# Kernel optimization log

Measured on AMD Instinct MI355X. Metric: run time of the kernel, lower is better.

Reference implementation:

```python
import jax, jax.numpy as jnp
import numpy as np

LN_EPS = 1e-5
B, N, D, V = 2048, 8, 1024, 4096


def setup_inputs() -> dict:
    key = jax.random.key(0)
    k1, k2, k3, k4 = jax.random.split(key, 4)
    return {
        "input_embedding": jax.random.normal(k1, (B, D), dtype=jnp.float32),
        "features": jax.random.randint(k2, (B, N), 0, V, dtype=jnp.int64),
        "embed_tables": jax.random.normal(k3, (N, V, D), dtype=jnp.float32) * 0.02,
        "W_pred": jax.random.normal(k4, (N, D, V), dtype=jnp.float32) * 0.02,
        "b_pred": jnp.zeros((N, V), dtype=jnp.float32),
        "ln_gamma": jnp.ones((D,), dtype=jnp.float32),
        "ln_beta": jnp.zeros((D,), dtype=jnp.float32),
    }


def reference(input_embedding, features, embed_tables, W_pred, b_pred, ln_gamma, ln_beta):
    # Per-feature embedding lookup: embed_tables[n, features[b,n]] -> [B, N, D]
    feat_emb = embed_tables[jnp.arange(N)[None, :], features]
    # Stack input embedding in front: [B, N+1, D]
    embeddings = jnp.concatenate([input_embedding[:, None, :], feat_emb], axis=1)
    # Original: triu(diag=1) mask-multiply-sum then [:, 1:, :].
    # masked_sums[:, t] = sum_{s < t} emb[:, s]; slicing t=1..N == inclusive cumsum
    # over the first N positions.
    masked_sums = jnp.cumsum(embeddings, axis=1)[:, :-1, :]  # [B, N, D]
    # LayerNorm over last dim
    mu = jnp.mean(masked_sums, axis=-1, keepdims=True)
    var = jnp.var(masked_sums, axis=-1, keepdims=True)
    h = (masked_sums - mu) / jnp.sqrt(var + LN_EPS) * ln_gamma + ln_beta
    # Exact (erf) GELU, matching nn.GELU default
    h = jax.nn.gelu(h, approximate=False)
    # Per-feature predictor heads as one batched GEMM: [B, N, V]
    logits = jnp.einsum("bnd,ndv->bnv", h, W_pred) + b_pred
    return logits
```

## Files before the change

### kernel.cpp

```cpp
#include <hip/hip_runtime.h>
#include <hip/hip_bf16.h>

#define B_ 2048
#define N_ 8
#define D_ 1024
#define V_ 4096
#define LN_EPS_ 1e-5f

typedef __bf16 bf16x8 __attribute__((ext_vector_type(8)));
typedef float f32x4 __attribute__((ext_vector_type(4)));

#define GLB(p) ((const __attribute__((address_space(1))) void*)(p))
#define LDSP(p) ((__attribute__((address_space(3))) void*)(p))

static __device__ __forceinline__ unsigned short f2bf(float x) {
    union { float f; unsigned int u; } v;
    v.f = x;
    unsigned int r = v.u + 0x7fffu + ((v.u >> 16) & 1u);
    return (unsigned short)(r >> 16);
}

__global__ __launch_bounds__(256) void wconv(const float* __restrict__ W,
                                             unsigned short* __restrict__ Wt) {
    __shared__ unsigned short tile[64][65];
    const int n  = blockIdx.z;
    const int v0 = blockIdx.x * 64;
    const int d0 = blockIdx.y * 64;
    const int tx = threadIdx.x;
    const int ty = threadIdx.y;
#pragma unroll
    for (int i = 0; i < 4; ++i) {
        const int d = ty + i * 16;
        const float4 w4 = *(const float4*)&W[((size_t)n * D_ + d0 + d) * V_ + v0 + tx * 4];
        tile[d][tx * 4 + 0] = f2bf(w4.x);
        tile[d][tx * 4 + 1] = f2bf(w4.y);
        tile[d][tx * 4 + 2] = f2bf(w4.z);
        tile[d][tx * 4 + 3] = f2bf(w4.w);
    }
    __syncthreads();
#pragma unroll
    for (int i = 0; i < 4; ++i) {
        const int v = ty + i * 16;
        ushort4 pk;
        pk.x = tile[tx * 4 + 0][v];
        pk.y = tile[tx * 4 + 1][v];
        pk.z = tile[tx * 4 + 2][v];
        pk.w = tile[tx * 4 + 3][v];
        *reinterpret_cast<ushort4*>(&Wt[((size_t)n * V_ + v0 + v) * D_ + d0 + tx * 4]) = pk;
    }
}

__global__ __launch_bounds__(256) void stage1(const float* __restrict__ ie,
                                              const int* __restrict__ feats,
                                              const float* __restrict__ emb,
                                              const float* __restrict__ gamma,
                                              const float* __restrict__ beta,
                                              unsigned short* __restrict__ H) {
    const int b = blockIdx.x;
    const int t = threadIdx.x;
    const int d0 = t * 4;
    const int lane = t & 63, wid = t >> 6;

    float4 s  = *(const float4*)&ie[(size_t)b * D_ + d0];
    const float4 g4 = *(const float4*)&gamma[d0];
    const float4 be4 = *(const float4*)&beta[d0];

    int fc[N_];
#pragma unroll
    for (int n = 0; n < N_; ++n) fc[n] = feats[b * N_ + n];

    __shared__ float redS[4], redQ[4];

#pragma unroll
    for (int n = 0; n < N_; ++n) {
        float ls = s.x + s.y + s.z + s.w;
        float lq = s.x * s.x + s.y * s.y + s.z * s.z + s.w * s.w;
#pragma unroll
        for (int off = 32; off > 0; off >>= 1) {
            ls += __shfl_down(ls, off, 64);
            lq += __shfl_down(lq, off, 64);
        }
        if (lane == 0) { redS[wid] = ls; redQ[wid] = lq; }
        __syncthreads();
        const float tot  = redS[0] + redS[1] + redS[2] + redS[3];
        const float totq = redQ[0] + redQ[1] + redQ[2] + redQ[3];
        __syncthreads();

        const float mu   = tot * (1.0f / D_);
        const float var  = totq * (1.0f / D_) - mu * mu;
        const float rstd = rsqrtf(var + LN_EPS_);

        float h0 = (s.x - mu) * rstd * g4.x + be4.x;
        float h1 = (s.y - mu) * rstd * g4.y + be4.y;
        float h2 = (s.z - mu) * rstd * g4.z + be4.z;
        float h3 = (s.w - mu) * rstd * g4.w + be4.w;
        h0 = 0.5f * h0 * (1.0f + erff(h0 * 0.70710678f));
        h1 = 0.5f * h1 * (1.0f + erff(h1 * 0.70710678f));
        h2 = 0.5f * h2 * (1.0f + erff(h2 * 0.70710678f));
        h3 = 0.5f * h3 * (1.0f + erff(h3 * 0.70710678f));

        ushort4 pk;
        pk.x = f2bf(h0); pk.y = f2bf(h1); pk.z = f2bf(h2); pk.w = f2bf(h3);
        *reinterpret_cast<ushort4*>(&H[((size_t)n * B_ + b) * D_ + d0]) = pk;

        const float4 e = *(const float4*)&emb[((size_t)n * V_ + fc[n]) * (size_t)D_ + d0];
        s.x += e.x; s.y += e.y; s.z += e.z; s.w += e.w;
    }
}

#define MF(a, b, c) __builtin_amdgcn_mfma_f32_16x16x32_bf16((a), (b), (c), 0, 0, 0)

#define STG_A(u, kt, bb) __builtin_amdgcn_global_load_lds( \
    GLB(Ab + (size_t)((u) * 64 + srow) * D_ + (kt) + gsl), \
    LDSP(lds + (bb) + (u) * 8192 + t * 16), 16, 0, 0)
#define STG_B(u, kt, bb) __builtin_amdgcn_global_load_lds( \
    GLB(Bb + (size_t)((u) * 64 + srow) * D_ + (kt) + gsl), \
    LDSP(lds + (bb) + 32768 + (u) * 8192 + t * 16), 16, 0, 0)

#define RD_A(i, ks, bb) (*(const bf16x8*)(lds + (bb) + ((i) >> 1) * 8192 + \
    (((i) & 1) * 32 + wr * 16 + lrow) * 128 + ((((ks) * 4 + lkq) ^ sw) * 16)))
#define RD_B(j, ks, bb) (*(const bf16x8*)(lds + (bb) + 32768 + wc * 8192 + \
    ((j) * 16 + lrow) * 128 + ((((ks) * 4 + lkq) ^ sw) * 16)))

#define QUADP(i0, i1) \
    _Pragma("unroll") for (int j = 0; j < 4; ++j) { \
        acc[i0][j] = MF(A00, Bf[j][0], acc[i0][j]); \
        acc[i0][j] = MF(A01, Bf[j][1], acc[i0][j]); \
        acc[i1][j] = MF(A10, Bf[j][0], acc[i1][j]); \
        acc[i1][j] = MF(A11, Bf[j][1], acc[i1][j]); \
    }

#define TILE(KT, bc, bn) { \
    bf16x8 Bf[4][2]; \
    asm volatile("s_waitcnt vmcnt(3)" ::: "memory"); \
    __builtin_amdgcn_s_barrier(); \
    _Pragma("unroll") for (int j = 0; j < 4; ++j) { Bf[j][0] = RD_B(j, 0, bc); Bf[j][1] = RD_B(j, 1, bc); } \
    { bf16x8 A00 = RD_A(0, 0, bc), A01 = RD_A(0, 1, bc), A10 = RD_A(1, 0, bc), A11 = RD_A(1, 1, bc); \
      STG_B(0, (KT) + 64, bn); STG_B(1, (KT) + 64, bn); \
      __builtin_amdgcn_s_setprio(1); QUADP(0, 1); __builtin_amdgcn_s_setprio(0); } \
    asm volatile("s_waitcnt vmcnt(4)" ::: "memory"); \
    __builtin_amdgcn_s_barrier(); \
    { bf16x8 A00 = RD_A(2, 0, bc), A01 = RD_A(2, 1, bc), A10 = RD_A(3, 0, bc), A11 = RD_A(3, 1, bc); \
      STG_B(2, (KT) + 64, bn); STG_B(3, (KT) + 64, bn); \
      __builtin_amdgcn_s_setprio(1); QUADP(2, 3); __builtin_amdgcn_s_setprio(0); } \
    asm volatile("s_waitcnt vmcnt(4)" ::: "memory"); \
    __builtin_amdgcn_s_barrier(); \
    { bf16x8 A00 = RD_A(4, 0, bc), A01 = RD_A(4, 1, bc), A10 = RD_A(5, 0, bc), A11 = RD_A(5, 1, bc); \
      STG_A(0, (KT) + 64, bn); STG_A(1, (KT) + 64, bn); \
      __builtin_amdgcn_s_setprio(1); QUADP(4, 5); __builtin_amdgcn_s_setprio(0); } \
    asm volatile("s_waitcnt vmcnt(6)" ::: "memory"); \
    __builtin_amdgcn_s_barrier(); \
    { bf16x8 A00 = RD_A(6, 0, bc), A01 = RD_A(6, 1, bc), A10 = RD_A(7, 0, bc), A11 = RD_A(7, 1, bc); \
      STG_A(2, (KT) + 64, bn); STG_A(3, (KT) + 64, bn); \
      __builtin_amdgcn_s_setprio(1); QUADP(6, 7); __builtin_amdgcn_s_setprio(0); } \
}

#define TILE_LAST(bc) { \
    bf16x8 Bf[4][2]; \
    asm volatile("s_waitcnt vmcnt(3)" ::: "memory"); \
    __builtin_amdgcn_s_barrier(); \
    _Pragma("unroll") for (int j = 0; j < 4; ++j) { Bf[j][0] = RD_B(j, 0, bc); Bf[j][1] = RD_B(j, 1, bc); } \
    { bf16x8 A00 = RD_A(0, 0, bc), A01 = RD_A(0, 1, bc), A10 = RD_A(1, 0, bc), A11 = RD_A(1, 1, bc); \
      __builtin_amdgcn_s_setprio(1); QUADP(0, 1); __builtin_amdgcn_s_setprio(0); } \
    asm volatile("s_waitcnt vmcnt(2)" ::: "memory"); \
    __builtin_amdgcn_s_barrier(); \
    { bf16x8 A00 = RD_A(2, 0, bc), A01 = RD_A(2, 1, bc), A10 = RD_A(3, 0, bc), A11 = RD_A(3, 1, bc); \
      __builtin_amdgcn_s_setprio(1); QUADP(2, 3); __builtin_amdgcn_s_setprio(0); } \
    asm volatile("s_waitcnt vmcnt(1)" ::: "memory"); \
    __builtin_amdgcn_s_barrier(); \
    { bf16x8 A00 = RD_A(4, 0, bc), A01 = RD_A(4, 1, bc), A10 = RD_A(5, 0, bc), A11 = RD_A(5, 1, bc); \
      __builtin_amdgcn_s_setprio(1); QUADP(4, 5); __builtin_amdgcn_s_setprio(0); } \
    asm volatile("s_waitcnt vmcnt(0)" ::: "memory"); \
    __builtin_amdgcn_s_barrier(); \
    { bf16x8 A00 = RD_A(6, 0, bc), A01 = RD_A(6, 1, bc), A10 = RD_A(7, 0, bc), A11 = RD_A(7, 1, bc); \
      __builtin_amdgcn_s_setprio(1); QUADP(6, 7); __builtin_amdgcn_s_setprio(0); } \
}

__global__ __launch_bounds__(512, 2) void gemm8(const unsigned short* __restrict__ H,
                                                const unsigned short* __restrict__ Wt,
                                                const float* __restrict__ bp,
                                                float* __restrict__ out) {
    extern __shared__ char lds[];
    const int vt = blockIdx.x, mt = blockIdx.y, n = blockIdx.z;
    const int t = threadIdx.x;
    const int wid = t >> 6, lane = t & 63;
    const int wr = wid >> 2, wc = wid & 3;

    const unsigned short* Ab = H  + ((size_t)n * B_ + (size_t)mt * 256) * D_;
    const unsigned short* Bb = Wt + ((size_t)n * V_ + (size_t)vt * 256) * D_;

    const int srow = t >> 3;
    const int gsl  = ((t & 7) ^ (srow & 7)) * 8;

    const int lrow = lane & 15;
    const int lkq  = lane >> 4;
    const int sw   = lane & 7;

    f32x4 acc[8][4] = {};

    STG_B(0, 0, 0); STG_B(1, 0, 0); STG_B(2, 0, 0); STG_B(3, 0, 0);
    STG_A(0, 0, 0); STG_A(1, 0, 0); STG_A(2, 0, 0); STG_A(3, 0, 0);

    int kt = 0;
#pragma unroll 1
    for (int it = 0; it < 7; ++it) {
        TILE(kt, 0, 65536); kt += 64;
        TILE(kt, 65536, 0); kt += 64;
    }
    TILE(kt, 0, 65536);
    TILE_LAST(65536);

    const int col = lane & 15;
    const int rg  = (lane >> 4) * 4;
    const int gc0 = vt * 256 + wc * 64 + col;
    float bias[4];
#pragma unroll
    for (int j = 0; j < 4; ++j) bias[j] = bp[(size_t)n * V_ + gc0 + j * 16];
#pragma unroll
    for (int i = 0; i < 8; ++i) {
        const int row = mt * 256 + i * 32 + wr * 16 + rg;
#pragma unroll
        for (int j = 0; j < 4; ++j) {
            const int gcol = gc0 + j * 16;
#pragma unroll
            for (int r = 0; r < 4; ++r) {
                out[((size_t)(row + r) * N_ + n) * V_ + gcol] = acc[i][j][r] + bias[j];
            }
        }
    }
}

extern "C" void kernel_launch(void* const* d_in, const int* in_sizes, int n_in,
                              void* d_out, int out_size, void* d_ws, size_t ws_size,
                              hipStream_t stream) {
    const float* ie  = (const float*)d_in[0];
    const int*   fts = (const int*)d_in[1];
    const float* emb = (const float*)d_in[2];
    const float* W   = (const float*)d_in[3];
    const float* bp  = (const float*)d_in[4];
    const float* gam = (const float*)d_in[5];
    const float* bet = (const float*)d_in[6];
    float* out = (float*)d_out;

    unsigned short* Wt = (unsigned short*)d_ws;
    unsigned short* H  = (unsigned short*)((char*)d_ws + (size_t)N_ * V_ * D_ * 2);

    (void)hipFuncSetAttribute(reinterpret_cast<const void*>(gemm8),
                              hipFuncAttributeMaxDynamicSharedMemorySize, 131072);

    wconv<<<dim3(V_ / 64, D_ / 64, N_), dim3(16, 16), 0, stream>>>(W, Wt);
    stage1<<<dim3(B_), dim3(256), 0, stream>>>(ie, fts, emb, gam, bet, H);
    gemm8<<<dim3(V_ / 256, B_ / 256, N_), 512, 131072, stream>>>(H, Wt, bp, out);
}
```

Baseline: 254.0 us.

## Merge prep kernels and make GEMM blocks persistent across four V tiles

Result: slower. 340.7 us (+34.1%).

```diff
diff --git a/kernel.cpp b/kernel.cpp
--- a/kernel.cpp
+++ b/kernel.cpp
@@ -20,101 +20,103 @@
     return (unsigned short)(r >> 16);
 }
 
-__global__ __launch_bounds__(256) void wconv(const float* __restrict__ W,
-                                             unsigned short* __restrict__ Wt) {
-    __shared__ unsigned short tile[64][65];
-    const int n  = blockIdx.z;
-    const int v0 = blockIdx.x * 64;
-    const int d0 = blockIdx.y * 64;
-    const int tx = threadIdx.x;
-    const int ty = threadIdx.y;
-#pragma unroll
-    for (int i = 0; i < 4; ++i) {
-        const int d = ty + i * 16;
-        const float4 w4 = *(const float4*)&W[((size_t)n * D_ + d0 + d) * V_ + v0 + tx * 4];
-        tile[d][tx * 4 + 0] = f2bf(w4.x);
-        tile[d][tx * 4 + 1] = f2bf(w4.y);
-        tile[d][tx * 4 + 2] = f2bf(w4.z);
-        tile[d][tx * 4 + 3] = f2bf(w4.w);
-    }
-    __syncthreads();
-#pragma unroll
-    for (int i = 0; i < 4; ++i) {
-        const int v = ty + i * 16;
-        ushort4 pk;
-        pk.x = tile[tx * 4 + 0][v];
-        pk.y = tile[tx * 4 + 1][v];
-        pk.z = tile[tx * 4 + 2][v];
-        pk.w = tile[tx * 4 + 3][v];
-        *reinterpret_cast<ushort4*>(&Wt[((size_t)n * V_ + v0 + v) * D_ + d0 + tx * 4]) = pk;
-    }
-}
-
-__global__ __launch_bounds__(256) void stage1(const float* __restrict__ ie,
-                                              const int* __restrict__ feats,
-                                              const float* __restrict__ emb,
-                                              const float* __restrict__ gamma,
-                                              const float* __restrict__ beta,
-                                              unsigned short* __restrict__ H) {
-    const int b = blockIdx.x;
+__global__ __launch_bounds__(256) void prep(const float* __restrict__ ie,
+                                            const int* __restrict__ feats,
+                                            const float* __restrict__ emb,
+                                            const float* __restrict__ gamma,
+                                            const float* __restrict__ beta,
+                                            const float* __restrict__ W,
+                                            unsigned short* __restrict__ H,
+                                            unsigned short* __restrict__ Wt) {
+    const int bid = blockIdx.x;
     const int t = threadIdx.x;
-    const int d0 = t * 4;
-    const int lane = t & 63, wid = t >> 6;
-
-    float4 s  = *(const float4*)&ie[(size_t)b * D_ + d0];
-    const float4 g4 = *(const float4*)&gamma[d0];
-    const float4 be4 = *(const float4*)&beta[d0];
-
-    int fc[N_];
-#pragma unroll
-    for (int n = 0; n < N_; ++n) fc[n] = feats[b * N_ + n];
-
-    __shared__ float redS[4], redQ[4];
-
-#pragma unroll
-    for (int n = 0; n < N_; ++n) {
-        float ls = s.x + s.y + s.z + s.w;
-        float lq = s.x * s.x + s.y * s.y + s.z * s.z + s.w * s.w;
-#pragma unroll
-        for (int off = 32; off > 0; off >>= 1) {
-            ls += __shfl_down(ls, off, 64);
-            lq += __shfl_down(lq, off, 64);
-        }
-        if (lane == 0) { redS[wid] = ls; redQ[wid] = lq; }
+
+    if (bid >= 2048) {
+        __shared__ unsigned short tile[64][65];
+        const int w  = bid - 2048;
+        const int v0 = (w & 63) * 64;
+        const int d0 = ((w >> 6) & 15) * 64;
+        const int n  = w >> 10;
+        const int tx = t & 15, ty = t >> 4;
+#pragma unroll
+        for (int i = 0; i < 4; ++i) {
+            const int d = ty + i * 16;
+            const float4 w4 = *(const float4*)&W[((size_t)n * D_ + d0 + d) * V_ + v0 + tx * 4];
+            tile[d][tx * 4 + 0] = f2bf(w4.x);
+            tile[d][tx * 4 + 1] = f2bf(w4.y);
+            tile[d][tx * 4 + 2] = f2bf(w4.z);
+            tile[d][tx * 4 + 3] = f2bf(w4.w);
+        }
         __syncthreads();
-        const float tot  = redS[0] + redS[1] + redS[2] + redS[3];
-        const float totq = redQ[0] + redQ[1] + redQ[2] + redQ[3];
-        __syncthreads();
-
-        const float mu   = tot * (1.0f / D_);
-        const float var  = totq * (1.0f / D_) - mu * mu;
-        const float rstd = rsqrtf(var + LN_EPS_);
-
-        float h0 = (s.x - mu) * rstd * g4.x + be4.x;
-        float h1 = (s.y - mu) * rstd * g4.y + be4.y;
-        float h2 = (s.z - mu) * rstd * g4.z + be4.z;
-        float h3 = (s.w - mu) * rstd * g4.w + be4.w;
-        h0 = 0.5f * h0 * (1.0f + erff(h0 * 0.70710678f));
-        h1 = 0.5f * h1 * (1.0f + erff(h1 * 0.70710678f));
-        h2 = 0.5f * h2 * (1.0f + erff(h2 * 0.70710678f));
-        h3 = 0.5f * h3 * (1.0f + erff(h3 * 0.70710678f));
-
-        ushort4 pk;
-        pk.x = f2bf(h0); pk.y = f2bf(h1); pk.z = f2bf(h2); pk.w = f2bf(h3);
-        *reinterpret_cast<ushort4*>(&H[((size_t)n * B_ + b) * D_ + d0]) = pk;
-
-        const float4 e = *(const float4*)&emb[((size_t)n * V_ + fc[n]) * (size_t)D_ + d0];
-        s.x += e.x; s.y += e.y; s.z += e.z; s.w += e.w;
+#pragma unroll
+        for (int i = 0; i < 4; ++i) {
+            const int v = ty + i * 16;
+            ushort4 pk;
+            pk.x = tile[tx * 4 + 0][v];
+            pk.y = tile[tx * 4 + 1][v];
+            pk.z = tile[tx * 4 + 2][v];
+            pk.w = tile[tx * 4 + 3][v];
+            *reinterpret_cast<ushort4*>(&Wt[((size_t)n * V_ + v0 + v) * D_ + d0 + tx * 4]) = pk;
+        }
+    } else {
+        __shared__ float redS[4], redQ[4];
+        const int b = bid;
+        const int d0 = t * 4;
+        const int lane = t & 63, wid = t >> 6;
+
+        float4 s  = *(const float4*)&ie[(size_t)b * D_ + d0];
+        const float4 g4 = *(const float4*)&gamma[d0];
+        const float4 be4 = *(const float4*)&beta[d0];
+
+        int fc[N_];
+#pragma unroll
+        for (int n = 0; n < N_; ++n) fc[n] = feats[b * N_ + n];
+
+#pragma unroll
+        for (int n = 0; n < N_; ++n) {
+            float ls = s.x + s.y + s.z + s.w;
+            float lq = s.x * s.x + s.y * s.y + s.z * s.z + s.w * s.w;
+#pragma unroll
+            for (int off = 32; off > 0; off >>= 1) {
+                ls += __shfl_down(ls, off, 64);
+                lq += __shfl_down(lq, off, 64);
+            }
+            if (lane == 0) { redS[wid] = ls; redQ[wid] = lq; }
+            __syncthreads();
+            const float tot  = redS[0] + redS[1] + redS[2] + redS[3];
+            const float totq = redQ[0] + redQ[1] + redQ[2] + redQ[3];
+            __syncthreads();
+
+            const float mu   = tot * (1.0f / D_);
+            const float var  = totq * (1.0f / D_) - mu * mu;
+            const float rstd = rsqrtf(var + LN_EPS_);
+
+            float h0 = (s.x - mu) * rstd * g4.x + be4.x;
+            float h1 = (s.y - mu) * rstd * g4.y + be4.y;
+            float h2 = (s.z - mu) * rstd * g4.z + be4.z;
+            float h3 = (s.w - mu) * rstd * g4.w + be4.w;
+            h0 = 0.5f * h0 * (1.0f + erff(h0 * 0.70710678f));
+            h1 = 0.5f * h1 * (1.0f + erff(h1 * 0.70710678f));
+            h2 = 0.5f * h2 * (1.0f + erff(h2 * 0.70710678f));
+            h3 = 0.5f * h3 * (1.0f + erff(h3 * 0.70710678f));
+
+            ushort4 pk;
+            pk.x = f2bf(h0); pk.y = f2bf(h1); pk.z = f2bf(h2); pk.w = f2bf(h3);
+            *reinterpret_cast<ushort4*>(&H[((size_t)n * B_ + b) * D_ + d0]) = pk;
+
+            const float4 e = *(const float4*)&emb[((size_t)n * V_ + fc[n]) * (size_t)D_ + d0];
+            s.x += e.x; s.y += e.y; s.z += e.z; s.w += e.w;
+        }
     }
 }
 
 #define MF(a, b, c) __builtin_amdgcn_mfma_f32_16x16x32_bf16((a), (b), (c), 0, 0, 0)
 
-#define STG_A(u, kt, bb) __builtin_amdgcn_global_load_lds( \
-    GLB(Ab + (size_t)((u) * 64 + srow) * D_ + (kt) + gsl), \
+#define STG_A(u, APTR, bb) __builtin_amdgcn_global_load_lds( \
+    GLB((APTR) + (size_t)((u) * 64 + srow) * D_ + gsl), \
     LDSP(lds + (bb) + (u) * 8192 + t * 16), 16, 0, 0)
-#define STG_B(u, kt, bb) __builtin_amdgcn_global_load_lds( \
-    GLB(Bb + (size_t)((u) * 64 + srow) * D_ + (kt) + gsl), \
+#define STG_B(u, BPTR, bb) __builtin_amdgcn_global_load_lds( \
+    GLB((BPTR) + (size_t)((u) * 64 + srow) * D_ + gsl), \
     LDSP(lds + (bb) + 32768 + (u) * 8192 + t * 16), 16, 0, 0)
 
 #define RD_A(i, ks, bb) (*(const bf16x8*)(lds + (bb) + ((i) >> 1) * 8192 + \
@@ -130,28 +132,28 @@
         acc[i1][j] = MF(A11, Bf[j][1], acc[i1][j]); \
     }
 
-#define TILE(KT, bc, bn) { \
+#define TILE(bc, bn, ANXT, BNXT) { \
     bf16x8 Bf[4][2]; \
     asm volatile("s_waitcnt vmcnt(3)" ::: "memory"); \
     __builtin_amdgcn_s_barrier(); \
     _Pragma("unroll") for (int j = 0; j < 4; ++j) { Bf[j][0] = RD_B(j, 0, bc); Bf[j][1] = RD_B(j, 1, bc); } \
     { bf16x8 A00 = RD_A(0, 0, bc), A01 = RD_A(0, 1, bc), A10 = RD_A(1, 0, bc), A11 = RD_A(1, 1, bc); \
-      STG_B(0, (KT) + 64, bn); STG_B(1, (KT) + 64, bn); \
+      STG_B(0, BNXT, bn); STG_B(1, BNXT, bn); \
       __builtin_amdgcn_s_setprio(1); QUADP(0, 1); __builtin_amdgcn_s_setprio(0); } \
     asm volatile("s_waitcnt vmcnt(4)" ::: "memory"); \
     __builtin_amdgcn_s_barrier(); \
     { bf16x8 A00 = RD_A(2, 0, bc), A01 = RD_A(2, 1, bc), A10 = RD_A(3, 0, bc), A11 = RD_A(3, 1, bc); \
-      STG_B(2, (KT) + 64, bn); STG_B(3, (KT) + 64, bn); \
+      STG_B(2, BNXT, bn); STG_B(3, BNXT, bn); \
       __builtin_amdgcn_s_setprio(1); QUADP(2, 3); __builtin_amdgcn_s_setprio(0); } \
     asm volatile("s_waitcnt vmcnt(4)" ::: "memory"); \
     __builtin_amdgcn_s_barrier(); \
     { bf16x8 A00 = RD_A(4, 0, bc), A01 = RD_A(4, 1, bc), A10 = RD_A(5, 0, bc), A11 = RD_A(5, 1, bc); \
-      STG_A(0, (KT) + 64, bn); STG_A(1, (KT) + 64, bn); \
+      STG_A(0, ANXT, bn); STG_A(1, ANXT, bn); \
       __builtin_amdgcn_s_setprio(1); QUADP(4, 5); __builtin_amdgcn_s_setprio(0); } \
     asm volatile("s_waitcnt vmcnt(6)" ::: "memory"); \
     __builtin_amdgcn_s_barrier(); \
     { bf16x8 A00 = RD_A(6, 0, bc), A01 = RD_A(6, 1, bc), A10 = RD_A(7, 0, bc), A11 = RD_A(7, 1, bc); \
-      STG_A(2, (KT) + 64, bn); STG_A(3, (KT) + 64, bn); \
+      STG_A(2, ANXT, bn); STG_A(3, ANXT, bn); \
       __builtin_amdgcn_s_setprio(1); QUADP(6, 7); __builtin_amdgcn_s_setprio(0); } \
 }
 
@@ -181,52 +183,78 @@
                                                 const float* __restrict__ bp,
                                                 float* __restrict__ out) {
     extern __shared__ char lds[];
-    const int vt = blockIdx.x, mt = blockIdx.y, n = blockIdx.z;
+    const int bid = blockIdx.x;
+    const int swz = (bid & 7) * 32 + (bid >> 3);
+    const int n   = swz >> 5;
+    const int mt  = (swz >> 2) & 7;
+    const int vtg = swz & 3;
+
     const int t = threadIdx.x;
     const int wid = t >> 6, lane = t & 63;
     const int wr = wid >> 2, wc = wid & 3;
 
     const unsigned short* Ab = H  + ((size_t)n * B_ + (size_t)mt * 256) * D_;
-    const unsigned short* Bb = Wt + ((size_t)n * V_ + (size_t)vt * 256) * D_;
+    const unsigned short* Bb = Wt + ((size_t)n * V_ + (size_t)vtg * 1024) * D_;
 
     const int srow = t >> 3;
     const int gsl  = ((t & 7) ^ (srow & 7)) * 8;
-
     const int lrow = lane & 15;
     const int lkq  = lane >> 4;
     const int sw   = lane & 7;
+    const int col  = lane & 15;
+    const int rg   = (lane >> 4) * 4;
+
+    f32x4 bias0, bias1, bias2, bias3;
+#pragma unroll
+    for (int j = 0; j < 4; ++j) {
+        const size_t bo = (size_t)n * V_ + (size_t)vtg * 1024 + wc * 64 + j * 16 + col;
+        bias0[j] = bp[bo];
+        bias1[j] = bp[bo + 256];
+        bias2[j] = bp[bo + 512];
+        bias3[j] = bp[bo + 768];
+    }
+    __builtin_amdgcn_sched_barrier(0);
 
     f32x4 acc[8][4] = {};
 
-    STG_B(0, 0, 0); STG_B(1, 0, 0); STG_B(2, 0, 0); STG_B(3, 0, 0);
-    STG_A(0, 0, 0); STG_A(1, 0, 0); STG_A(2, 0, 0); STG_A(3, 0, 0);
-
-    int kt = 0;
+    STG_B(0, Bb, 0); STG_B(1, Bb, 0); STG_B(2, Bb, 0); STG_B(3, Bb, 0);
+    STG_A(0, Ab, 0); STG_A(1, Ab, 0); STG_A(2, Ab, 0); STG_A(3, Ab, 0);
+
+    const unsigned short* Bc = Bb;
 #pragma unroll 1
-    for (int it = 0; it < 7; ++it) {
-        TILE(kt, 0, 65536); kt += 64;
-        TILE(kt, 65536, 0); kt += 64;
-    }
-    TILE(kt, 0, 65536);
-    TILE_LAST(65536);
-
-    const int col = lane & 15;
-    const int rg  = (lane >> 4) * 4;
-    const int gc0 = vt * 256 + wc * 64 + col;
-    float bias[4];
-#pragma unroll
-    for (int j = 0; j < 4; ++j) bias[j] = bp[(size_t)n * V_ + gc0 + j * 16];
-#pragma unroll
-    for (int i = 0; i < 8; ++i) {
-        const int row = mt * 256 + i * 32 + wr * 16 + rg;
-#pragma unroll
-        for (int j = 0; j < 4; ++j) {
-            const int gcol = gc0 + j * 16;
-#pragma unroll
-            for (int r = 0; r < 4; ++r) {
-                out[((size_t)(row + r) * N_ + n) * V_ + gcol] = acc[i][j][r] + bias[j];
+    for (int it = 0; it < 4; ++it) {
+        const unsigned short* Bn = Bc + (size_t)256 * D_;
+#pragma unroll 1
+        for (int lt2 = 0; lt2 < 7; ++lt2) {
+            const int k0 = lt2 * 128;
+            TILE(0, 65536, Ab + k0 + 64, Bc + k0 + 64);
+            TILE(65536, 0, Ab + k0 + 128, Bc + k0 + 128);
+        }
+        TILE(0, 65536, Ab + 960, Bc + 960);
+        if (it < 3) { TILE(65536, 0, Ab, Bn); }
+        else        { TILE_LAST(65536); }
+
+        const int gc0 = (vtg * 4 + it) * 256 + wc * 64 + col;
+        const f32x4 bs = (it == 0) ? bias0 : (it == 1) ? bias1 : (it == 2) ? bias2 : bias3;
+#pragma unroll
+        for (int i = 0; i < 8; ++i) {
+            const int row = mt * 256 + i * 32 + wr * 16 + rg;
+#pragma unroll
+            for (int j = 0; j < 4; ++j) {
+                const int gcol = gc0 + j * 16;
+#pragma unroll
+                for (int r = 0; r < 4; ++r)
+                    out[((size_t)(row + r) * N_ + n) * V_ + gcol] = acc[i][j][r] + bs[j];
             }
         }
+        if (it < 3) {
+#pragma unroll
+            for (int i = 0; i < 8; ++i)
+#pragma unroll
+                for (int j = 0; j < 4; ++j)
+                    acc[i][j] = (f32x4){0.f, 0.f, 0.f, 0.f};
+        }
+        Bc = Bn;
     }
 }
 
@@ -248,7 +276,6 @@
     (void)hipFuncSetAttribute(reinterpret_cast<const void*>(gemm8),
                               hipFuncAttributeMaxDynamicSharedMemorySize, 131072);
 
-    wconv<<<dim3(V_ / 64, D_ / 64, N_), dim3(16, 16), 0, stream>>>(W, Wt);
-    stage1<<<dim3(B_), dim3(256), 0, stream>>>(ie, fts, emb, gam, bet, H);
-    gemm8<<<dim3(V_ / 256, B_ / 256, N_), 512, 131072, stream>>>(H, Wt, bp, out);
-}
+    prep<<<dim3(2048 + 8192), dim3(256), 0, stream>>>(ie, fts, emb, gam, bet, W, H, Wt);
+    gemm8<<<dim3(256), dim3(512), 131072, stream>>>(H, Wt, bp, out);
+}
```

## Merge weight conversion and LN/GELU prep into one launch; add GEMM barriers

Applied to the files above, without the earlier changes.

After: 232.4 us. 8.5% less time.

```diff
diff --git a/kernel.cpp b/kernel.cpp
--- a/kernel.cpp
+++ b/kernel.cpp
@@ -20,91 +20,93 @@
     return (unsigned short)(r >> 16);
 }
 
-__global__ __launch_bounds__(256) void wconv(const float* __restrict__ W,
-                                             unsigned short* __restrict__ Wt) {
-    __shared__ unsigned short tile[64][65];
-    const int n  = blockIdx.z;
-    const int v0 = blockIdx.x * 64;
-    const int d0 = blockIdx.y * 64;
-    const int tx = threadIdx.x;
-    const int ty = threadIdx.y;
-#pragma unroll
-    for (int i = 0; i < 4; ++i) {
-        const int d = ty + i * 16;
-        const float4 w4 = *(const float4*)&W[((size_t)n * D_ + d0 + d) * V_ + v0 + tx * 4];
-        tile[d][tx * 4 + 0] = f2bf(w4.x);
-        tile[d][tx * 4 + 1] = f2bf(w4.y);
-        tile[d][tx * 4 + 2] = f2bf(w4.z);
-        tile[d][tx * 4 + 3] = f2bf(w4.w);
-    }
-    __syncthreads();
-#pragma unroll
-    for (int i = 0; i < 4; ++i) {
-        const int v = ty + i * 16;
-        ushort4 pk;
-        pk.x = tile[tx * 4 + 0][v];
-        pk.y = tile[tx * 4 + 1][v];
-        pk.z = tile[tx * 4 + 2][v];
-        pk.w = tile[tx * 4 + 3][v];
-        *reinterpret_cast<ushort4*>(&Wt[((size_t)n * V_ + v0 + v) * D_ + d0 + tx * 4]) = pk;
-    }
-}
-
-__global__ __launch_bounds__(256) void stage1(const float* __restrict__ ie,
-                                              const int* __restrict__ feats,
-                                              const float* __restrict__ emb,
-                                              const float* __restrict__ gamma,
-                                              const float* __restrict__ beta,
-                                              unsigned short* __restrict__ H) {
-    const int b = blockIdx.x;
+__global__ __launch_bounds__(256) void prep(const float* __restrict__ ie,
+                                            const int* __restrict__ feats,
+                                            const float* __restrict__ emb,
+                                            const float* __restrict__ gamma,
+                                            const float* __restrict__ beta,
+                                            const float* __restrict__ W,
+                                            unsigned short* __restrict__ H,
+                                            unsigned short* __restrict__ Wt) {
+    const int bid = blockIdx.x;
     const int t = threadIdx.x;
-    const int d0 = t * 4;
-    const int lane = t & 63, wid = t >> 6;
-
-    float4 s  = *(const float4*)&ie[(size_t)b * D_ + d0];
-    const float4 g4 = *(const float4*)&gamma[d0];
-    const float4 be4 = *(const float4*)&beta[d0];
-
-    int fc[N_];
-#pragma unroll
-    for (int n = 0; n < N_; ++n) fc[n] = feats[b * N_ + n];
-
-    __shared__ float redS[4], redQ[4];
-
-#pragma unroll
-    for (int n = 0; n < N_; ++n) {
-        float ls = s.x + s.y + s.z + s.w;
-        float lq = s.x * s.x + s.y * s.y + s.z * s.z + s.w * s.w;
-#pragma unroll
-        for (int off = 32; off > 0; off >>= 1) {
-            ls += __shfl_down(ls, off, 64);
-            lq += __shfl_down(lq, off, 64);
-        }
-        if (lane == 0) { redS[wid] = ls; redQ[wid] = lq; }
+
+    if (bid >= 2048) {
+        __shared__ unsigned short tile[64][65];
+        const int w  = bid - 2048;
+        const int v0 = (w & 63) * 64;
+        const int d0 = ((w >> 6) & 15) * 64;
+        const int n  = w >> 10;
+        const int tx = t & 15, ty = t >> 4;
+#pragma unroll
+        for (int i = 0; i < 4; ++i) {
+            const int d = ty + i * 16;
+            const float4 w4 = *(const float4*)&W[((size_t)n * D_ + d0 + d) * V_ + v0 + tx * 4];
+            tile[d][tx * 4 + 0] = f2bf(w4.x);
+            tile[d][tx * 4 + 1] = f2bf(w4.y);
+            tile[d][tx * 4 + 2] = f2bf(w4.z);
+            tile[d][tx * 4 + 3] = f2bf(w4.w);
+        }
         __syncthreads();
-        const float tot  = redS[0] + redS[1] + redS[2] + redS[3];
-        const float totq = redQ[0] + redQ[1] + redQ[2] + redQ[3];
-        __syncthreads();
-
-        const float mu   = tot * (1.0f / D_);
-        const float var  = totq * (1.0f / D_) - mu * mu;
-        const float rstd = rsqrtf(var + LN_EPS_);
-
-        float h0 = (s.x - mu) * rstd * g4.x + be4.x;
-        float h1 = (s.y - mu) * rstd * g4.y + be4.y;
-        float h2 = (s.z - mu) * rstd * g4.z + be4.z;
-        float h3 = (s.w - mu) * rstd * g4.w + be4.w;
-        h0 = 0.5f * h0 * (1.0f + erff(h0 * 0.70710678f));
-        h1 = 0.5f * h1 * (1.0f + erff(h1 * 0.70710678f));
-        h2 = 0.5f * h2 * (1.0f + erff(h2 * 0.70710678f));
-        h3 = 0.5f * h3 * (1.0f + erff(h3 * 0.70710678f));
-
-        ushort4 pk;
-        pk.x = f2bf(h0); pk.y = f2bf(h1); pk.z = f2bf(h2); pk.w = f2bf(h3);
-        *reinterpret_cast<ushort4*>(&H[((size_t)n * B_ + b) * D_ + d0]) = pk;
-
-        const float4 e = *(const float4*)&emb[((size_t)n * V_ + fc[n]) * (size_t)D_ + d0];
-        s.x += e.x; s.y += e.y; s.z += e.z; s.w += e.w;
+#pragma unroll
+        for (int i = 0; i < 4; ++i) {
+            const int v = ty + i * 16;
+            ushort4 pk;
+            pk.x = tile[tx * 4 + 0][v];
+            pk.y = tile[tx * 4 + 1][v];
+            pk.z = tile[tx * 4 + 2][v];
+            pk.w = tile[tx * 4 + 3][v];
+            *reinterpret_cast<ushort4*>(&Wt[((size_t)n * V_ + v0 + v) * D_ + d0 + tx * 4]) = pk;
+        }
+    } else {
+        __shared__ float redS[4], redQ[4];
+        const int b = bid;
+        const int d0 = t * 4;
+        const int lane = t & 63, wid = t >> 6;
+
+        float4 s  = *(const float4*)&ie[(size_t)b * D_ + d0];
+        const float4 g4 = *(const float4*)&gamma[d0];
+        const float4 be4 = *(const float4*)&beta[d0];
+
+        int fc[N_];
+#pragma unroll
+        for (int n = 0; n < N_; ++n) fc[n] = feats[b * N_ + n];
+
+#pragma unroll
+        for (int n = 0; n < N_; ++n) {
+            float ls = s.x + s.y + s.z + s.w;
+            float lq = s.x * s.x + s.y * s.y + s.z * s.z + s.w * s.w;
+#pragma unroll
+            for (int off = 32; off > 0; off >>= 1) {
+                ls += __shfl_down(ls, off, 64);
+                lq += __shfl_down(lq, off, 64);
+            }
+            if (lane == 0) { redS[wid] = ls; redQ[wid] = lq; }
+            __syncthreads();
+            const float tot  = redS[0] + redS[1] + redS[2] + redS[3];
+            const float totq = redQ[0] + redQ[1] + redQ[2] + redQ[3];
+            __syncthreads();
+
+            const float mu   = tot * (1.0f / D_);
+            const float var  = totq * (1.0f / D_) - mu * mu;
+            const float rstd = rsqrtf(var + LN_EPS_);
+
+            float h0 = (s.x - mu) * rstd * g4.x + be4.x;
+            float h1 = (s.y - mu) * rstd * g4.y + be4.y;
+            float h2 = (s.z - mu) * rstd * g4.z + be4.z;
+            float h3 = (s.w - mu) * rstd * g4.w + be4.w;
+            h0 = 0.5f * h0 * (1.0f + erff(h0 * 0.70710678f));
+            h1 = 0.5f * h1 * (1.0f + erff(h1 * 0.70710678f));
+            h2 = 0.5f * h2 * (1.0f + erff(h2 * 0.70710678f));
+            h3 = 0.5f * h3 * (1.0f + erff(h3 * 0.70710678f));
+
+            ushort4 pk;
+            pk.x = f2bf(h0); pk.y = f2bf(h1); pk.z = f2bf(h2); pk.w = f2bf(h3);
+            *reinterpret_cast<ushort4*>(&H[((size_t)n * B_ + b) * D_ + d0]) = pk;
+
+            const float4 e = *(const float4*)&emb[((size_t)n * V_ + fc[n]) * (size_t)D_ + d0];
+            s.x += e.x; s.y += e.y; s.z += e.z; s.w += e.w;
+        }
     }
 }
 
@@ -138,21 +140,25 @@
     { bf16x8 A00 = RD_A(0, 0, bc), A01 = RD_A(0, 1, bc), A10 = RD_A(1, 0, bc), A11 = RD_A(1, 1, bc); \
       STG_B(0, (KT) + 64, bn); STG_B(1, (KT) + 64, bn); \
       __builtin_amdgcn_s_setprio(1); QUADP(0, 1); __builtin_amdgcn_s_setprio(0); } \
+    __builtin_amdgcn_s_barrier(); \
     asm volatile("s_waitcnt vmcnt(4)" ::: "memory"); \
     __builtin_amdgcn_s_barrier(); \
     { bf16x8 A00 = RD_A(2, 0, bc), A01 = RD_A(2, 1, bc), A10 = RD_A(3, 0, bc), A11 = RD_A(3, 1, bc); \
       STG_B(2, (KT) + 64, bn); STG_B(3, (KT) + 64, bn); \
       __builtin_amdgcn_s_setprio(1); QUADP(2, 3); __builtin_amdgcn_s_setprio(0); } \
+    __builtin_amdgcn_s_barrier(); \
     asm volatile("s_waitcnt vmcnt(4)" ::: "memory"); \
     __builtin_amdgcn_s_barrier(); \
     { bf16x8 A00 = RD_A(4, 0, bc), A01 = RD_A(4, 1, bc), A10 = RD_A(5, 0, bc), A11 = RD_A(5, 1, bc); \
       STG_A(0, (KT) + 64, bn); STG_A(1, (KT) + 64, bn); \
       __builtin_amdgcn_s_setprio(1); QUADP(4, 5); __builtin_amdgcn_s_setprio(0); } \
+    __builtin_amdgcn_s_barrier(); \
     asm volatile("s_waitcnt vmcnt(6)" ::: "memory"); \
     __builtin_amdgcn_s_barrier(); \
     { bf16x8 A00 = RD_A(6, 0, bc), A01 = RD_A(6, 1, bc), A10 = RD_A(7, 0, bc), A11 = RD_A(7, 1, bc); \
       STG_A(2, (KT) + 64, bn); STG_A(3, (KT) + 64, bn); \
       __builtin_amdgcn_s_setprio(1); QUADP(6, 7); __builtin_amdgcn_s_setprio(0); } \
+    __builtin_amdgcn_s_barrier(); \
 }
 
 #define TILE_LAST(bc) { \
@@ -162,14 +168,17 @@
     _Pragma("unroll") for (int j = 0; j < 4; ++j) { Bf[j][0] = RD_B(j, 0, bc); Bf[j][1] = RD_B(j, 1, bc); } \
     { bf16x8 A00 = RD_A(0, 0, bc), A01 = RD_A(0, 1, bc), A10 = RD_A(1, 0, bc), A11 = RD_A(1, 1, bc); \
       __builtin_amdgcn_s_setprio(1); QUADP(0, 1); __builtin_amdgcn_s_setprio(0); } \
+    __builtin_amdgcn_s_barrier(); \
     asm volatile("s_waitcnt vmcnt(2)" ::: "memory"); \
     __builtin_amdgcn_s_barrier(); \
     { bf16x8 A00 = RD_A(2, 0, bc), A01 = RD_A(2, 1, bc), A10 = RD_A(3, 0, bc), A11 = RD_A(3, 1, bc); \
       __builtin_amdgcn_s_setprio(1); QUADP(2, 3); __builtin_amdgcn_s_setprio(0); } \
+    __builtin_amdgcn_s_barrier(); \
     asm volatile("s_waitcnt vmcnt(1)" ::: "memory"); \
     __builtin_amdgcn_s_barrier(); \
     { bf16x8 A00 = RD_A(4, 0, bc), A01 = RD_A(4, 1, bc), A10 = RD_A(5, 0, bc), A11 = RD_A(5, 1, bc); \
       __builtin_amdgcn_s_setprio(1); QUADP(4, 5); __builtin_amdgcn_s_setprio(0); } \
+    __builtin_amdgcn_s_barrier(); \
     asm volatile("s_waitcnt vmcnt(0)" ::: "memory"); \
     __builtin_amdgcn_s_barrier(); \
     { bf16x8 A00 = RD_A(6, 0, bc), A01 = RD_A(6, 1, bc), A10 = RD_A(7, 0, bc), A11 = RD_A(7, 1, bc); \
@@ -191,10 +200,17 @@
 
     const int srow = t >> 3;
     const int gsl  = ((t & 7) ^ (srow & 7)) * 8;
-
     const int lrow = lane & 15;
     const int lkq  = lane >> 4;
     const int sw   = lane & 7;
+
+    const int col = lane & 15;
+    float bias[4];
+#pragma unroll
+    for (int j = 0; j < 4; ++j)
+        bias[j] = bp[(size_t)n * V_ + vt * 256 + wc * 64 + j * 16 + col];
+    asm volatile("s_waitcnt vmcnt(0)" ::: "memory");
+    __builtin_amdgcn_sched_barrier(0);
 
     f32x4 acc[8][4] = {};
 
@@ -210,12 +226,8 @@
     TILE(kt, 0, 65536);
     TILE_LAST(65536);
 
-    const int col = lane & 15;
     const int rg  = (lane >> 4) * 4;
     const int gc0 = vt * 256 + wc * 64 + col;
-    float bias[4];
-#pragma unroll
-    for (int j = 0; j < 4; ++j) bias[j] = bp[(size_t)n * V_ + gc0 + j * 16];
 #pragma unroll
     for (int i = 0; i < 8; ++i) {
         const int row = mt * 256 + i * 32 + wr * 16 + rg;
@@ -248,7 +260,6 @@
     (void)hipFuncSetAttribute(reinterpret_cast<const void*>(gemm8),
                               hipFuncAttributeMaxDynamicSharedMemorySize, 131072);
 
-    wconv<<<dim3(V_ / 64, D_ / 64, N_), dim3(16, 16), 0, stream>>>(W, Wt);
-    stage1<<<dim3(B_), dim3(256), 0, stream>>>(ie, fts, emb, gam, bet, H);
-    gemm8<<<dim3(V_ / 256, B_ / 256, N_), 512, 131072, stream>>>(H, Wt, bp, out);
-}
+    prep<<<dim3(2048 + 8192), dim3(256), 0, stream>>>(ie, fts, emb, gam, bet, W, H, Wt);
+    gemm8<<<dim3(V_ / 256, B_ / 256, N_), dim3(512), 131072, stream>>>(H, Wt, bp, out);
+}
```
